# Kernel optimization log

Measured on AMD Instinct MI355X. Metric: run time of the kernel, lower is better.

## Reference

```python
import jax, jax.numpy as jnp
import numpy as np

D_MODEL = 1024
N_HEADS = 16
HEAD_DIM = D_MODEL // N_HEADS


def setup_inputs() -> dict:
    key = jax.random.key(0)
    k1, k2, k3 = jax.random.split(key, 3)
    x = jax.random.normal(k1, (2, 2048, D_MODEL), dtype=jnp.float32)
    w_qkv = jax.random.normal(k2, (3 * D_MODEL, D_MODEL), dtype=jnp.float32) * 0.02
    w_out = jax.random.normal(k3, (D_MODEL, D_MODEL), dtype=jnp.float32) * 0.02
    return {"x": x, "w_qkv": w_qkv, "w_out": w_out}


def reference(x, w_qkv, w_out):
    B, T, D = x.shape
    H, Hd = N_HEADS, HEAD_DIM
    # QKV projection: Linear stores weight as [out, in] -> '...i,oi->...o'
    qkv = jnp.einsum('bti,oi->bto', x, w_qkv)              # [B, T, 3D]
    # split (3*H, Hs) group-major, chunk into q/k/v of H heads each
    qkv = qkv.reshape(B, T, 3, H, Hd)
    q = jnp.transpose(qkv[:, :, 0], (0, 2, 1, 3))          # [B, H, T, Hd]
    k = jnp.transpose(qkv[:, :, 1], (0, 2, 1, 3))
    v = jnp.transpose(qkv[:, :, 2], (0, 2, 1, 3))
    scale = 1.0 / jnp.sqrt(jnp.asarray(Hd, dtype=x.dtype))
    scores = jnp.einsum('bhqd,bhkd->bhqk', q, k) * scale   # [B, H, T, T]
    causal = jnp.tril(jnp.ones((T, T), dtype=bool))        # [T, T]
    scores = jnp.where(causal[None, None], scores, jnp.asarray(-jnp.inf, dtype=scores.dtype))
    attn = jax.nn.softmax(scores, axis=-1)
    ctx = jnp.einsum('bhqk,bhkd->bhqd', attn, v)           # [B, H, T, Hd]
    ctx = jnp.transpose(ctx, (0, 2, 1, 3)).reshape(B, T, D)
    return jnp.einsum('bti,oi->bto', ctx, w_out)
```

## Files before the change

kernel.cpp:

```cpp
#include <hip/hip_runtime.h>


typedef short short8 __attribute__((ext_vector_type(8)));
typedef float f32x4 __attribute__((ext_vector_type(4)));
typedef unsigned short u16;
typedef unsigned int u32;

#define T_SEQ 2048
#define N_B 2
#define N_H 16
#define HD 64
#define DM 1024
#define TRIPLE 3072

__device__ __forceinline__ u16 f2bf(float f) {
  union { float f; unsigned u; } v;
  v.f = f;
  unsigned r = v.u + 0x7fffu + ((v.u >> 16) & 1u);
  return (u16)(r >> 16);
}

__device__ __forceinline__ float bf2f(u16 x) {
  return __uint_as_float((u32)x << 16);
}

__device__ __forceinline__ u32 cvtpk(float a, float b) {
  u32 r;
  asm("v_cvt_pk_bf16_f32 %0, %1, %2" : "=v"(r) : "v"(a), "v"(b));
  return r;
}

typedef const __attribute__((address_space(1))) void gvoid;
typedef __attribute__((address_space(3))) void lvoid;

__device__ __forceinline__ void g2l16(const void* g, void* l) {
  __builtin_amdgcn_global_load_lds((gvoid*)g, (lvoid*)l, 16, 0, 0);
}

__device__ __forceinline__ void storeC(float* p, float v) { *p = v; }
__device__ __forceinline__ void storeC(u16* p, float v) { *p = f2bf(v); }

__global__ __launch_bounds__(256) void cast_all(const float4* __restrict__ x,
                                                const float4* __restrict__ wq,
                                                const float4* __restrict__ wo,
                                                ushort4* __restrict__ out) {
  int i = blockIdx.x * 256 + threadIdx.x;
  const float4* src;
  int off;
  if (i < 1048576) { src = x; off = 0; }
  else if (i < 1835008) { src = wq; off = 1048576; }
  else { src = wo; off = 1835008; }
  float4 v = src[i - off];
  ushort4 o;
  o.x = f2bf(v.x); o.y = f2bf(v.y); o.z = f2bf(v.z); o.w = f2bf(v.w);
  out[i] = o;
}

__global__ __launch_bounds__(256) void vtrans(const u16* __restrict__ qkv,
                                              u16* __restrict__ vT) {
  const int tid = threadIdx.x;
  const int w = tid >> 6, lane = tid & 63;
  const int ti = lane >> 3, di = lane & 7;
  const int h = blockIdx.y, b = blockIdx.z;
  const int t0 = blockIdx.x * 256 + w * 64 + ti * 8;

  const u16* src = qkv + (size_t)(b * T_SEQ + t0) * TRIPLE + 2 * DM + h * HD + di * 8;
  u32 x[8][4];
#pragma unroll
  for (int e = 0; e < 8; ++e) {
    union { short8 v; u32 u[4]; } cv;
    cv.v = *(const short8*)(src + (size_t)e * TRIPLE);
#pragma unroll
    for (int j = 0; j < 4; ++j) x[e][j] = cv.u[j];
  }
  u32 y[8][4];
#pragma unroll
  for (int a = 0; a < 4; ++a)
#pragma unroll
    for (int j = 0; j < 4; ++j) {
      u32 lo = x[2 * a][j], hi = x[2 * a + 1][j];
      y[2 * a][j] = (lo & 0x0000FFFFu) | (hi << 16);
      y[2 * a + 1][j] = (lo >> 16) | (hi & 0xFFFF0000u);
    }
  u16* dst = vT + ((size_t)(b * N_H + h) * HD + di * 8) * T_SEQ + t0;
#pragma unroll
  for (int dd = 0; dd < 8; ++dd) {
    union { short8 v; u32 u[4]; } cv;
#pragma unroll
    for (int a = 0; a < 4; ++a) cv.u[a] = y[2 * a + (dd & 1)][dd >> 1];
    *(short8*)(dst + (size_t)dd * T_SEQ) = cv.v;
  }
}

template <typename OutT>
__global__ __launch_bounds__(256) void gemm_bt(const u16* __restrict__ A,
                                               const u16* __restrict__ W,
                                               OutT* __restrict__ C,
                                               int M, int N, int K) {
  __shared__ char As[128 * 64 * 2];
  __shared__ char Bs[128 * 64 * 2];
  const int tid = threadIdx.x;
  const int lane = tid & 63, w = tid >> 6;
  const int l15 = lane & 15, l4 = lane >> 4;
  const int m0 = blockIdx.y * 128, n0 = blockIdx.x * 128;
  const int wr = (w >> 1) * 64, wc = (w & 1) * 64;

  const f32x4 zero = {0.f, 0.f, 0.f, 0.f};
  f32x4 acc[4][4];
#pragma unroll
  for (int m = 0; m < 4; ++m)
#pragma unroll
    for (int n = 0; n < 4; ++n) acc[m][n] = zero;

  for (int k0 = 0; k0 < K; k0 += 64) {
#pragma unroll
    for (int i = 0; i < 4; ++i) {
      const int cb = (i * 4 + w) * 64;
      const int c = cb + lane;
      const int row = c >> 3;
      const int ks = ((c & 7) ^ (row & 7)) * 8;
      g2l16(A + (size_t)(m0 + row) * K + k0 + ks, As + (size_t)cb * 16);
      g2l16(W + (size_t)(n0 + row) * K + k0 + ks, Bs + (size_t)cb * 16);
    }
    __syncthreads();

#pragma unroll
    for (int kk = 0; kk < 2; ++kk) {
      short8 a[4], b[4];
#pragma unroll
      for (int m = 0; m < 4; ++m) {
        int row = wr + m * 16 + l15;
        int slot = (kk * 4 + l4) ^ (row & 7);
        a[m] = *(const short8*)(As + row * 128 + slot * 16);
      }
#pragma unroll
      for (int n = 0; n < 4; ++n) {
        int row = wc + n * 16 + l15;
        int slot = (kk * 4 + l4) ^ (row & 7);
        b[n] = *(const short8*)(Bs + row * 128 + slot * 16);
      }
#pragma unroll
      for (int m = 0; m < 4; ++m)
#pragma unroll
        for (int n = 0; n < 4; ++n)
          acc[m][n] = __builtin_amdgcn_mfma_f32_16x16x32_bf16(a[m], b[n], acc[m][n], 0, 0, 0);
    }
    __syncthreads();
  }

#pragma unroll
  for (int m = 0; m < 4; ++m)
#pragma unroll
    for (int n = 0; n < 4; ++n)
#pragma unroll
      for (int r = 0; r < 4; ++r) {
        int row = m0 + wr + m * 16 + l4 * 4 + r;
        int col = n0 + wc + n * 16 + l15;
        storeC(C + (size_t)row * N + col, acc[m][n][r]);
      }
}

__global__ __launch_bounds__(256) void attn_fwd(const u16* __restrict__ qkv,
                                                const u16* __restrict__ vT,
                                                u16* __restrict__ ctx) {
  __shared__ char Ks[2][8192];
  __shared__ char Vs[2][8192];
  __shared__ char Pl[4][2048];

  const int tid = threadIdx.x;
  const int lane = tid & 63, w = tid >> 6;
  const int l15 = lane & 15, l4 = lane >> 4;
  const int h = blockIdx.y, b = blockIdx.z;
  const int g = h + N_H * b;
  const int p = blockIdx.x;
  const int q0A = 64 * p, q0B = 64 * (31 - p);

  const float c_log2 = 0.18033688011112042f;
  short8 qa2[2][2];
#pragma unroll
  for (int ps = 0; ps < 2; ++ps) {
    const int qq0 = ps ? q0B : q0A;
    const u16* qp = qkv + (size_t)(b * T_SEQ + qq0 + w * 16 + l15) * TRIPLE + h * HD;
#pragma unroll
    for (int kk = 0; kk < 2; ++kk) {
      short8 raw = *(const short8*)(qp + kk * 32 + l4 * 8);
      union { short8 v; u32 w4[4]; } qq;
#pragma unroll
      for (int j = 0; j < 4; ++j)
        qq.w4[j] = cvtpk(bf2f((u16)raw[2 * j]) * c_log2,
                         bf2f((u16)raw[2 * j + 1]) * c_log2);
      qa2[ps][kk] = qq.v;
    }
  }

  const int r0 = tid >> 3, c0 = tid & 7;
  const int swz = (c0 ^ (r0 & 7)) << 3;
  const u16* kbase = qkv + (size_t)(b * T_SEQ + r0) * TRIPLE + DM + h * HD + swz;
  const u16* vbase = vT + ((size_t)g * HD + r0) * T_SEQ + swz;

#define STAGE(kt_, buf_)                                                        \
  {                                                                             \
    g2l16(kbase + (size_t)((kt_) * 64) * TRIPLE, Ks[buf_] + tid * 16);          \
    g2l16(kbase + (size_t)((kt_) * 64 + 32) * TRIPLE, Ks[buf_] + tid * 16 + 4096); \
    g2l16(vbase + (kt_) * 64, Vs[buf_] + tid * 16);                             \
    g2l16(vbase + (size_t)32 * T_SEQ + (kt_) * 64, Vs[buf_] + tid * 16 + 4096); \
  }

  char* Plb = Pl[w];

  const f32x4 zero = {0.f, 0.f, 0.f, 0.f};
  f32x4 o[4];
#pragma unroll
  for (int nt = 0; nt < 4; ++nt) o[nt] = zero;
  float mr = -INFINITY, lr = 0.f;
  short8 qa0 = qa2[0][0], qa1 = qa2[0][1];
  int q0 = q0A;

  STAGE(0, 0);
  __syncthreads();
  int cur = 0;

  for (int i = 0;; ++i) {
    const int kt = (i <= p) ? i : 32 - i;

    if (i < 32) {
      const int nkt = (i < p) ? i + 1 : 31 - i;
      STAGE(nkt, cur ^ 1);
    }

    f32x4 s[4];
#pragma unroll
    for (int mt = 0; mt < 4; ++mt) s[mt] = zero;
    __builtin_amdgcn_s_setprio(1);
#pragma unroll
    for (int mt = 0; mt < 4; ++mt) {
      int row = mt * 16 + l15;
      int slot0 = l4 ^ (row & 7);
      short8 kb0 = *(const short8*)(Ks[cur] + row * 128 + slot0 * 16);
      s[mt] = __builtin_amdgcn_mfma_f32_16x16x32_bf16(kb0, qa0, s[mt], 0, 0, 0);
      int slot1 = (4 + l4) ^ (row & 7);
      short8 kb1 = *(const short8*)(Ks[cur] + row * 128 + slot1 * 16);
      s[mt] = __builtin_amdgcn_mfma_f32_16x16x32_bf16(kb1, qa1, s[mt], 0, 0, 0);
    }
    __builtin_amdgcn_s_setprio(0);

    if (i == p || i == p + 1) {
      const int qrow = q0 + w * 16 + l15;
#pragma unroll
      for (int mt = 0; mt < 4; ++mt)
#pragma unroll
        for (int r = 0; r < 4; ++r) {
          int key = kt * 64 + mt * 16 + l4 * 4 + r;
          if (key > qrow) s[mt][r] = -INFINITY;
        }
    }

    float mx = fmaxf(fmaxf(fmaxf(s[0][0], s[0][1]), fmaxf(s[0][2], s[0][3])),
                     fmaxf(fmaxf(s[1][0], s[1][1]), fmaxf(s[1][2], s[1][3])));
    mx = fmaxf(mx, fmaxf(fmaxf(fmaxf(s[2][0], s[2][1]), fmaxf(s[2][2], s[2][3])),
                         fmaxf(fmaxf(s[3][0], s[3][1]), fmaxf(s[3][2], s[3][3]))));
    mx = fmaxf(mx, __shfl_xor(mx, 16));
    mx = fmaxf(mx, __shfl_xor(mx, 32));
    if (!__all(mx - mr <= 8.0f)) {
      float mn = fmaxf(mr, mx);
      float fr = exp2f(mr - mn);
      lr *= fr;
#pragma unroll
      for (int r = 0; r < 4; ++r) {
        float frq = __shfl(fr, l4 * 4 + r);
#pragma unroll
        for (int nt = 0; nt < 4; ++nt) o[nt][r] *= frq;
      }
      mr = mn;
    }
    float ps = 0.f;
#pragma unroll
    for (int mt = 0; mt < 4; ++mt)
#pragma unroll
      for (int r = 0; r < 4; ++r) {
        float pv = exp2f(s[mt][r] - mr);
        s[mt][r] = pv;
        ps += pv;
      }
    lr += ps;

#pragma unroll
    for (int mt = 0; mt < 4; ++mt) {
      uint2 pw;
      pw.x = cvtpk(s[mt][0], s[mt][1]);
      pw.y = cvtpk(s[mt][2], s[mt][3]);
      int slot = ((mt * 2 + (l4 >> 1)) ^ (l15 & 7));
      *(uint2*)(Plb + l15 * 128 + (slot << 4) + ((l4 & 1) << 3)) = pw;
    }

    __builtin_amdgcn_s_setprio(1);
#pragma unroll
    for (int kk = 0; kk < 2; ++kk) {
      short8 pa = *(const short8*)(Plb + l15 * 128 + (((kk * 4 + l4) ^ (l15 & 7)) << 4));
#pragma unroll
      for (int nt = 0; nt < 4; ++nt) {
        int d = nt * 16 + l15;
        int slot = (kk * 4 + l4) ^ (l15 & 7);
        short8 vb = *(const short8*)(Vs[cur] + d * 128 + slot * 16);
        o[nt] = __builtin_amdgcn_mfma_f32_16x16x32_bf16(pa, vb, o[nt], 0, 0, 0);
      }
    }
    __builtin_amdgcn_s_setprio(0);

    if (i == p) {
      lr += __shfl_xor(lr, 16);
      lr += __shfl_xor(lr, 32);
#pragma unroll
      for (int r = 0; r < 4; ++r) {
        float lrq = __shfl(lr, l4 * 4 + r);
        float inv = __builtin_amdgcn_rcpf(lrq);
        size_t t = (size_t)(b * T_SEQ + q0A + w * 16 + l4 * 4 + r);
#pragma unroll
        for (int nt = 0; nt < 4; ++nt)
          ctx[t * DM + h * HD + nt * 16 + l15] = f2bf(o[nt][r] * inv);
      }
#pragma unroll
      for (int nt = 0; nt < 4; ++nt) o[nt] = zero;
      mr = -INFINITY; lr = 0.f;
      qa0 = qa2[1][0]; qa1 = qa2[1][1];
      q0 = q0B;
    } else if (i == 32) {
      lr += __shfl_xor(lr, 16);
      lr += __shfl_xor(lr, 32);
#pragma unroll
      for (int r = 0; r < 4; ++r) {
        float lrq = __shfl(lr, l4 * 4 + r);
        float inv = __builtin_amdgcn_rcpf(lrq);
        size_t t = (size_t)(b * T_SEQ + q0B + w * 16 + l4 * 4 + r);
#pragma unroll
        for (int nt = 0; nt < 4; ++nt)
          ctx[t * DM + h * HD + nt * 16 + l15] = f2bf(o[nt][r] * inv);
      }
      break;
    }

    __syncthreads();
    cur ^= 1;
  }
#undef STAGE
}

extern "C" void kernel_launch(void* const* d_in, const int* in_sizes, int n_in,
                              void* d_out, int out_size, void* d_ws, size_t ws_size,
                              hipStream_t stream) {
  const float* x = (const float*)d_in[0];
  const float* wqkv = (const float*)d_in[1];
  const float* wout = (const float*)d_in[2];
  float* out = (float*)d_out;
  char* ws = (char*)d_ws;

  u16* xb    = (u16*)(ws);
  u16* wqkvb = (u16*)(ws + 8u * 1024 * 1024);
  u16* woutb = (u16*)(ws + 14u * 1024 * 1024);
  u16* qkvb  = (u16*)(ws + 16u * 1024 * 1024);
  u16* ctxb  = (u16*)(ws + 40u * 1024 * 1024);
  u16* vTb   = (u16*)(ws + 48u * 1024 * 1024);

  cast_all<<<8192, 256, 0, stream>>>((const float4*)x, (const float4*)wqkv,
                                     (const float4*)wout, (ushort4*)xb);

  gemm_bt<u16><<<dim3(24, 32), 256, 0, stream>>>(xb, wqkvb, qkvb, 4096, 3072, 1024);

  vtrans<<<dim3(8, N_H, N_B), 256, 0, stream>>>(qkvb, vTb);

  attn_fwd<<<dim3(16, N_H, N_B), 256, 0, stream>>>(qkvb, vTb, ctxb);

  gemm_bt<float><<<dim3(8, 32), 256, 0, stream>>>(ctxb, woutb, out, 4096, 1024, 1024);
}
```

Baseline: 132.2 us.

## Widen attention blocks to 8 waves with triple-buffered K/V prefetch

The attention kernel now runs 512 threads per block and covers 128 query rows per pass, so each K/V tile loaded into LDS is shared by twice as many waves. Staging moves to a three-buffer ring that prefetches two tiles ahead, with explicit vmcnt waits and barriers replacing __syncthreads. Waves whose query rows lie entirely before a key tile skip that tile's compute. The grid is reordered so head and batch vary fastest. The cost is halving the block count to 256, which lowers occupancy and parallelism, and raising per-block LDS use.

```diff
diff --git a/kernel.cpp b/kernel.cpp
--- a/kernel.cpp
+++ b/kernel.cpp
@@ -160,20 +160,21 @@
       }
 }
 
-__global__ __launch_bounds__(256) void attn_fwd(const u16* __restrict__ qkv,
+__global__ __launch_bounds__(512) void attn_fwd(const u16* __restrict__ qkv,
                                                 const u16* __restrict__ vT,
                                                 u16* __restrict__ ctx) {
-  __shared__ char Ks[2][8192];
-  __shared__ char Vs[2][8192];
-  __shared__ char Pl[4][2048];
+  __shared__ char Ks[3][8192];
+  __shared__ char Vs[3][8192];
+  __shared__ char Pl[8][2048];
 
   const int tid = threadIdx.x;
   const int lane = tid & 63, w = tid >> 6;
   const int l15 = lane & 15, l4 = lane >> 4;
-  const int h = blockIdx.y, b = blockIdx.z;
-  const int g = h + N_H * b;
-  const int p = blockIdx.x;
-  const int q0A = 64 * p, q0B = 64 * (31 - p);
+  const int g = blockIdx.x;
+  const int p = blockIdx.y;
+  const int h = g & 15, b = g >> 4;
+  const int q0A = 128 * p, q0B = 128 * (15 - p);
+  const int nA = 2 * p + 2;
 
   const float c_log2 = 0.18033688011112042f;
   short8 qa2[2][2];
@@ -198,12 +199,10 @@
   const u16* kbase = qkv + (size_t)(b * T_SEQ + r0) * TRIPLE + DM + h * HD + swz;
   const u16* vbase = vT + ((size_t)g * HD + r0) * T_SEQ + swz;
 
-#define STAGE(kt_, buf_)                                                        \
-  {                                                                             \
-    g2l16(kbase + (size_t)((kt_) * 64) * TRIPLE, Ks[buf_] + tid * 16);          \
-    g2l16(kbase + (size_t)((kt_) * 64 + 32) * TRIPLE, Ks[buf_] + tid * 16 + 4096); \
-    g2l16(vbase + (kt_) * 64, Vs[buf_] + tid * 16);                             \
-    g2l16(vbase + (size_t)32 * T_SEQ + (kt_) * 64, Vs[buf_] + tid * 16 + 4096); \
+#define STAGE(kt_, buf_)                                                     \
+  {                                                                          \
+    g2l16(kbase + (size_t)((kt_) * (64 * TRIPLE)), Ks[buf_] + tid * 16);     \
+    g2l16(vbase + (u32)((kt_) * 64), Vs[buf_] + tid * 16);                   \
   }
 
   char* Plb = Pl[w];
@@ -217,130 +216,127 @@
   int q0 = q0A;
 
   STAGE(0, 0);
-  __syncthreads();
+  STAGE(1, 1);
+  asm volatile("s_waitcnt vmcnt(2)\n\ts_barrier" ::: "memory");
+
   int cur = 0;
-
   for (int i = 0;; ++i) {
-    const int kt = (i <= p) ? i : 32 - i;
-
-    if (i < 32) {
-      const int nkt = (i < p) ? i + 1 : 31 - i;
-      STAGE(nkt, cur ^ 1);
-    }
-
-    f32x4 s[4];
-#pragma unroll
-    for (int mt = 0; mt < 4; ++mt) s[mt] = zero;
-    __builtin_amdgcn_s_setprio(1);
-#pragma unroll
-    for (int mt = 0; mt < 4; ++mt) {
-      int row = mt * 16 + l15;
-      int slot0 = l4 ^ (row & 7);
-      short8 kb0 = *(const short8*)(Ks[cur] + row * 128 + slot0 * 16);
-      s[mt] = __builtin_amdgcn_mfma_f32_16x16x32_bf16(kb0, qa0, s[mt], 0, 0, 0);
-      int slot1 = (4 + l4) ^ (row & 7);
-      short8 kb1 = *(const short8*)(Ks[cur] + row * 128 + slot1 * 16);
-      s[mt] = __builtin_amdgcn_mfma_f32_16x16x32_bf16(kb1, qa1, s[mt], 0, 0, 0);
-    }
-    __builtin_amdgcn_s_setprio(0);
-
-    if (i == p || i == p + 1) {
-      const int qrow = q0 + w * 16 + l15;
+    const int kt = (i < nA) ? i : 33 - i;
+
+    if (i + 2 < 34) {
+      const int kt2 = (i + 2 < nA) ? (i + 2) : 31 - i;
+      int sb = cur - 1;
+      if (sb < 0) sb = 2;
+      STAGE(kt2, sb);
+    }
+
+    const int k0 = kt * 64;
+    if (k0 <= q0 + w * 16) {
+      f32x4 s[4];
+#pragma unroll
+      for (int mt = 0; mt < 4; ++mt) s[mt] = zero;
+      __builtin_amdgcn_s_setprio(1);
+#pragma unroll
+      for (int mt = 0; mt < 4; ++mt) {
+        int row = mt * 16 + l15;
+        int slot0 = l4 ^ (row & 7);
+        short8 kb0 = *(const short8*)(Ks[cur] + row * 128 + slot0 * 16);
+        s[mt] = __builtin_amdgcn_mfma_f32_16x16x32_bf16(kb0, qa0, s[mt], 0, 0, 0);
+        int slot1 = (4 + l4) ^ (row & 7);
+        short8 kb1 = *(const short8*)(Ks[cur] + row * 128 + slot1 * 16);
+        s[mt] = __builtin_amdgcn_mfma_f32_16x16x32_bf16(kb1, qa1, s[mt], 0, 0, 0);
+      }
+      __builtin_amdgcn_s_setprio(0);
+
+      if (i >= nA - 2 && i <= nA + 1) {
+        const int qrow = q0 + w * 16 + l15;
+#pragma unroll
+        for (int mt = 0; mt < 4; ++mt)
+#pragma unroll
+          for (int r = 0; r < 4; ++r) {
+            int key = k0 + mt * 16 + l4 * 4 + r;
+            if (key > qrow) s[mt][r] = -INFINITY;
+          }
+      }
+
+      float mx = fmaxf(fmaxf(fmaxf(s[0][0], s[0][1]), fmaxf(s[0][2], s[0][3])),
+                       fmaxf(fmaxf(s[1][0], s[1][1]), fmaxf(s[1][2], s[1][3])));
+      mx = fmaxf(mx, fmaxf(fmaxf(fmaxf(s[2][0], s[2][1]), fmaxf(s[2][2], s[2][3])),
+                           fmaxf(fmaxf(s[3][0], s[3][1]), fmaxf(s[3][2], s[3][3]))));
+      mx = fmaxf(mx, __shfl_xor(mx, 16));
+      mx = fmaxf(mx, __shfl_xor(mx, 32));
+      if (!__all(mx - mr <= 8.0f)) {
+        float mn = fmaxf(mr, mx);
+        float fr = exp2f(mr - mn);
+        lr *= fr;
+#pragma unroll
+        for (int r = 0; r < 4; ++r) {
+          float frq = __shfl(fr, l4 * 4 + r);
+#pragma unroll
+          for (int nt = 0; nt < 4; ++nt) o[nt][r] *= frq;
+        }
+        mr = mn;
+      }
+      float ps = 0.f;
 #pragma unroll
       for (int mt = 0; mt < 4; ++mt)
 #pragma unroll
         for (int r = 0; r < 4; ++r) {
-          int key = kt * 64 + mt * 16 + l4 * 4 + r;
-          if (key > qrow) s[mt][r] = -INFINITY;
+          float pv = exp2f(s[mt][r] - mr);
+          s[mt][r] = pv;
+          ps += pv;
         }
-    }
-
-    float mx = fmaxf(fmaxf(fmaxf(s[0][0], s[0][1]), fmaxf(s[0][2], s[0][3])),
-                     fmaxf(fmaxf(s[1][0], s[1][1]), fmaxf(s[1][2], s[1][3])));
-    mx = fmaxf(mx, fmaxf(fmaxf(fmaxf(s[2][0], s[2][1]), fmaxf(s[2][2], s[2][3])),
-                         fmaxf(fmaxf(s[3][0], s[3][1]), fmaxf(s[3][2], s[3][3]))));
-    mx = fmaxf(mx, __shfl_xor(mx, 16));
-    mx = fmaxf(mx, __shfl_xor(mx, 32));
-    if (!__all(mx - mr <= 8.0f)) {
-      float mn = fmaxf(mr, mx);
-      float fr = exp2f(mr - mn);
-      lr *= fr;
-#pragma unroll
-      for (int r = 0; r < 4; ++r) {
-        float frq = __shfl(fr, l4 * 4 + r);
-#pragma unroll
-        for (int nt = 0; nt < 4; ++nt) o[nt][r] *= frq;
-      }
-      mr = mn;
-    }
-    float ps = 0.f;
-#pragma unroll
-    for (int mt = 0; mt < 4; ++mt)
-#pragma unroll
-      for (int r = 0; r < 4; ++r) {
-        float pv = exp2f(s[mt][r] - mr);
-        s[mt][r] = pv;
-        ps += pv;
-      }
-    lr += ps;
-
-#pragma unroll
-    for (int mt = 0; mt < 4; ++mt) {
-      uint2 pw;
-      pw.x = cvtpk(s[mt][0], s[mt][1]);
-      pw.y = cvtpk(s[mt][2], s[mt][3]);
-      int slot = ((mt * 2 + (l4 >> 1)) ^ (l15 & 7));
-      *(uint2*)(Plb + l15 * 128 + (slot << 4) + ((l4 & 1) << 3)) = pw;
-    }
-
-    __builtin_amdgcn_s_setprio(1);
-#pragma unroll
-    for (int kk = 0; kk < 2; ++kk) {
-      short8 pa = *(const short8*)(Plb + l15 * 128 + (((kk * 4 + l4) ^ (l15 & 7)) << 4));
-#pragma unroll
-      for (int nt = 0; nt < 4; ++nt) {
-        int d = nt * 16 + l15;
-        int slot = (kk * 4 + l4) ^ (l15 & 7);
-        short8 vb = *(const short8*)(Vs[cur] + d * 128 + slot * 16);
-        o[nt] = __builtin_amdgcn_mfma_f32_16x16x32_bf16(pa, vb, o[nt], 0, 0, 0);
-      }
-    }
-    __builtin_amdgcn_s_setprio(0);
-
-    if (i == p) {
+      lr += ps;
+
+#pragma unroll
+      for (int mt = 0; mt < 4; ++mt) {
+        uint2 pw;
+        pw.x = cvtpk(s[mt][0], s[mt][1]);
+        pw.y = cvtpk(s[mt][2], s[mt][3]);
+        int slot = ((mt * 2 + (l4 >> 1)) ^ (l15 & 7));
+        *(uint2*)(Plb + l15 * 128 + (slot << 4) + ((l4 & 1) << 3)) = pw;
+      }
+
+      __builtin_amdgcn_s_setprio(1);
+#pragma unroll
+      for (int kk = 0; kk < 2; ++kk) {
+        short8 pa = *(const short8*)(Plb + l15 * 128 + (((kk * 4 + l4) ^ (l15 & 7)) << 4));
+#pragma unroll
+        for (int nt = 0; nt < 4; ++nt) {
+          int d = nt * 16 + l15;
+          int slot = (kk * 4 + l4) ^ (l15 & 7);
+          short8 vb = *(const short8*)(Vs[cur] + d * 128 + slot * 16);
+          o[nt] = __builtin_amdgcn_mfma_f32_16x16x32_bf16(pa, vb, o[nt], 0, 0, 0);
+        }
+      }
+      __builtin_amdgcn_s_setprio(0);
+    }
+
+    if (i == nA - 1 || i == 33) {
       lr += __shfl_xor(lr, 16);
       lr += __shfl_xor(lr, 32);
 #pragma unroll
       for (int r = 0; r < 4; ++r) {
         float lrq = __shfl(lr, l4 * 4 + r);
         float inv = __builtin_amdgcn_rcpf(lrq);
-        size_t t = (size_t)(b * T_SEQ + q0A + w * 16 + l4 * 4 + r);
+        size_t t = (size_t)(b * T_SEQ + q0 + w * 16 + l4 * 4 + r);
 #pragma unroll
         for (int nt = 0; nt < 4; ++nt)
           ctx[t * DM + h * HD + nt * 16 + l15] = f2bf(o[nt][r] * inv);
       }
+      if (i == 33) break;
 #pragma unroll
       for (int nt = 0; nt < 4; ++nt) o[nt] = zero;
       mr = -INFINITY; lr = 0.f;
       qa0 = qa2[1][0]; qa1 = qa2[1][1];
       q0 = q0B;
-    } else if (i == 32) {
-      lr += __shfl_xor(lr, 16);
-      lr += __shfl_xor(lr, 32);
-#pragma unroll
-      for (int r = 0; r < 4; ++r) {
-        float lrq = __shfl(lr, l4 * 4 + r);
-        float inv = __builtin_amdgcn_rcpf(lrq);
-        size_t t = (size_t)(b * T_SEQ + q0B + w * 16 + l4 * 4 + r);
-#pragma unroll
-        for (int nt = 0; nt < 4; ++nt)
-          ctx[t * DM + h * HD + nt * 16 + l15] = f2bf(o[nt][r] * inv);
-      }
-      break;
-    }
-
-    __syncthreads();
-    cur ^= 1;
+    }
+
+    if (i == 32)
+      asm volatile("s_waitcnt vmcnt(0)\n\ts_barrier" ::: "memory");
+    else
+      asm volatile("s_waitcnt vmcnt(2)\n\ts_barrier" ::: "memory");
+    cur = (cur == 2) ? 0 : cur + 1;
   }
 #undef STAGE
 }
@@ -368,7 +364,7 @@
 
   vtrans<<<dim3(8, N_H, N_B), 256, 0, stream>>>(qkvb, vTb);
 
-  attn_fwd<<<dim3(16, N_H, N_B), 256, 0, stream>>>(qkvb, vTb, ctxb);
+  attn_fwd<<<dim3(32, 8), 512, 0, stream>>>(qkvb, vTb, ctxb);
 
   gemm_bt<float><<<dim3(8, 32), 256, 0, stream>>>(ctxb, woutb, out, 4096, 1024, 1024);
 }
```

After: 126.9 us. 1.04x faster.
